# Performance work log

Measured on AMD Instinct MI355X. Metric: run time of the kernel, lower is better.

The kernel has to match this reference:

```python
import jax, jax.numpy as jnp
import numpy as np

# Deformable Aggregation (DAF) core of Sparse4DHead1st:
# multi-camera, multi-level bilinear point sampling + grouped weighted reduction.
# feature:            [bs, num_cams, sum(H_l*W_l), C]
# spatial_shapes:     [num_levels, 2] (H, W) per level (static metadata)
# level_start_index:  [num_levels] offsets into the flattened HW axis
# points_2d:          [bs, num_anchor, num_pts, num_cams, 2] normalized (x, y) in [0, 1]
# weights:            [bs, num_anchor, num_pts, num_cams, num_levels, num_groups]
# output:             [bs, num_anchor, C]  (sum over pts, cams, levels)

BS, CAMS, C = 1, 6, 256
NUM_ANCHOR, NUM_PTS = 900, 13
NUM_LEVELS, NUM_GROUPS = 4, 8
LEVEL_SHAPES = np.array([[64, 176], [32, 88], [16, 44], [8, 22]], np.int32)


def setup_inputs() -> dict:
    key = jax.random.key(0)
    k1, k2, k3 = jax.random.split(key, 3)
    hw = LEVEL_SHAPES[:, 0] * LEVEL_SHAPES[:, 1]
    starts = np.concatenate([[0], np.cumsum(hw)[:-1]]).astype(np.int32)
    total = int(hw.sum())  # 14960
    feature = jax.random.normal(k1, (BS, CAMS, total, C), jnp.float32)
    points_2d = jax.random.uniform(k2, (BS, NUM_ANCHOR, NUM_PTS, CAMS, 2), jnp.float32)
    # learned attention weights (normalized-ish so outputs stay O(1))
    weights = jax.random.uniform(
        k3, (BS, NUM_ANCHOR, NUM_PTS, CAMS, NUM_LEVELS, NUM_GROUPS), jnp.float32
    ) / (NUM_PTS * CAMS * NUM_LEVELS)
    return {
        "feature": feature,
        "spatial_shapes": jnp.asarray(LEVEL_SHAPES),
        "level_start_index": jnp.asarray(starts),
        "points_2d": points_2d,
        "weights": weights,
    }


def reference(feature, spatial_shapes, level_start_index, points_2d, weights):
    # spatial shapes / starts are static metadata (control slicing sizes)
    shapes = np.asarray(spatial_shapes)
    starts = np.asarray(level_start_index)
    bs, cams, _, c = feature.shape
    _, A, P, _, _ = points_2d.shape
    L, G = weights.shape[-2], weights.shape[-1]
    gc = c // G  # channels per group
    rowids = jnp.arange(bs * cams)[:, None]

    px = points_2d[..., 0]  # [bs, A, P, cams], normalized x
    py = points_2d[..., 1]

    out = jnp.zeros((bs, A, G, gc), feature.dtype)
    for l in range(L):
        h, w = int(shapes[l, 0]), int(shapes[l, 1])
        s = int(starts[l])
        feat = feature[:, :, s : s + h * w, :].reshape(bs * cams, h * w, c)
        x = px * w - 0.5
        y = py * h - 0.5
        x0 = jnp.floor(x)
        y0 = jnp.floor(y)
        bil = 0.0
        for dx in (0, 1):
            for dy in (0, 1):
                xi = x0 + dx
                yi = y0 + dy
                cw = (1.0 - jnp.abs(x - xi)) * (1.0 - jnp.abs(y - yi))
                valid = (xi >= 0) & (xi < w) & (yi >= 0) & (yi < h)
                idx = (jnp.clip(yi, 0, h - 1) * w + jnp.clip(xi, 0, w - 1)).astype(jnp.int32)
                # [bs, A, P, cams] -> [bs*cams, A*P]
                idx = idx.transpose(0, 3, 1, 2).reshape(bs * cams, A * P)
                cwm = (cw * valid).transpose(0, 3, 1, 2).reshape(bs * cams, A * P)
                v = feat[rowids, idx]  # gather: [bs*cams, A*P, C]
                bil = bil + v * cwm[..., None]
        bil = bil.reshape(bs, cams, A, P, G, gc)
        out = out + jnp.einsum("bcapgd,bapcg->bagd", bil, weights[..., l, :])
    return out.reshape(bs, A, c)
```

## Files before the change

kernel.cpp:

```cpp
#include <hip/hip_runtime.h>

#define NA 900
#define NP 13
#define NCAM 6
#define NL 4
#define NG 8
#define NC 256
#define TOTALHW 14960
#define NPC (NP * NCAM)
#define NS (NPC * NL)
#define NW 8

__device__ __constant__ int c_h[NL]  = {64, 32, 16, 8};
__device__ __constant__ int c_w[NL]  = {176, 88, 44, 22};
__device__ __constant__ int c_st[NL] = {0, 11264, 14080, 14784};

__global__ __launch_bounds__(512) void daf_kernel(
    const float* __restrict__ feature,
    const int* __restrict__ spatial_shapes,
    const int* __restrict__ level_start,
    const float* __restrict__ points,
    const float* __restrict__ weights,
    float* __restrict__ out)
{
    const int a    = blockIdx.x;
    const int tid  = threadIdx.x;
    const int wv   = tid >> 6;
    const int lane = tid & 63;

    __shared__ int    s_idx[NS][4];
    __shared__ float  s_cw[NS][4];
    __shared__ float  s_wg[NS * NG];
    __shared__ float4 s_part[NW][64];

    const float* wsrc = weights + (size_t)a * NS * NG;
    for (int i = tid; i < NS * NG; i += 512) {
        const int g  = i & (NG - 1);
        const int s  = i >> 3;
        const int l  = s / NPC;
        const int pc = s - l * NPC;
        s_wg[i] = wsrc[(pc * NL + l) * NG + g];
    }

    if (tid < NS) {
        const int s   = tid;
        const int l   = s / NPC;
        const int pc  = s - l * NPC;
        const int cam = pc % NCAM;
        const int p   = pc / NCAM;

        const float2 pt = *(const float2*)(points + (((size_t)a * NP + p) * NCAM + cam) * 2);
        const int h  = c_h[l];
        const int w  = c_w[l];
        const int st = c_st[l];

        const float x   = pt.x * (float)w - 0.5f;
        const float y   = pt.y * (float)h - 0.5f;
        const float x0f = floorf(x);
        const float y0f = floorf(y);
        const int   x0  = (int)x0f;
        const int   y0  = (int)y0f;
        const float fx  = x - x0f;
        const float fy  = y - y0f;
        const float wx[2] = {1.0f - fx, fx};
        const float wy[2] = {1.0f - fy, fy};

        const int base = cam * TOTALHW + st;
        #pragma unroll
        for (int k = 0; k < 4; ++k) {
            const int dx = k & 1;
            const int dy = k >> 1;
            const int xi = x0 + dx;
            const int yi = y0 + dy;
            const bool valid = (xi >= 0) && (xi < w) && (yi >= 0) && (yi < h);
            const int xc = min(max(xi, 0), w - 1);
            const int yc = min(max(yi, 0), h - 1);
            s_idx[s][k] = base + yc * w + xc;
            s_cw[s][k]  = valid ? wx[dx] * wy[dy] : 0.0f;
        }
    }
    __syncthreads();

    const int g = lane >> 3;
    const float4* __restrict__ f4 = (const float4*)feature;

    float4 acc = make_float4(0.f, 0.f, 0.f, 0.f);
    for (int s = wv; s < NS; s += NW) {
        const float wg = s_wg[s * NG + g];
        const int   i0 = s_idx[s][0], i1 = s_idx[s][1], i2 = s_idx[s][2], i3 = s_idx[s][3];
        const float c0 = s_cw[s][0] * wg, c1 = s_cw[s][1] * wg;
        const float c2 = s_cw[s][2] * wg, c3 = s_cw[s][3] * wg;

        const float4 v0 = f4[(size_t)i0 * 64 + lane];
        const float4 v1 = f4[(size_t)i1 * 64 + lane];
        const float4 v2 = f4[(size_t)i2 * 64 + lane];
        const float4 v3 = f4[(size_t)i3 * 64 + lane];

        acc.x += v0.x * c0 + v1.x * c1 + v2.x * c2 + v3.x * c3;
        acc.y += v0.y * c0 + v1.y * c1 + v2.y * c2 + v3.y * c3;
        acc.z += v0.z * c0 + v1.z * c1 + v2.z * c2 + v3.z * c3;
        acc.w += v0.w * c0 + v1.w * c1 + v2.w * c2 + v3.w * c3;
    }

    s_part[wv][lane] = acc;
    __syncthreads();

    if (tid < 64) {
        float4 r = s_part[0][lane];
        #pragma unroll
        for (int k = 1; k < NW; ++k) {
            const float4 p = s_part[k][lane];
            r.x += p.x; r.y += p.y; r.z += p.z; r.w += p.w;
        }
        ((float4*)out)[(size_t)a * 64 + lane] = r;
    }
}

extern "C" void kernel_launch(void* const* d_in, const int* in_sizes, int n_in,
                              void* d_out, int out_size, void* d_ws, size_t ws_size,
                              hipStream_t stream) {
    const float* feature        = (const float*)d_in[0];
    const int*   spatial_shapes = (const int*)d_in[1];
    const int*   level_start    = (const int*)d_in[2];
    const float* points         = (const float*)d_in[3];
    const float* weights        = (const float*)d_in[4];
    float*       out            = (float*)d_out;

    daf_kernel<<<NA, 512, 0, stream>>>(feature, spatial_shapes, level_start,
                                       points, weights, out);
}
```

Measured before the change: 214.5 us.

## Convert features to bf16 in workspace before gather-reduce kernel

Adds a pre-pass that converts the whole fp32 feature tensor to bf16 in the workspace, and a gather kernel that reads half-width bf16 rows and accumulates in fp32. The gather loop is also unrolled by two. The intent is to halve the bytes moved by the random bilinear gathers. The price is an extra full read of the feature tensor plus a half-size write on every call, and reduced precision in the sampled values. The fp32 kernel is kept as a fallback when the workspace is too small.

New measurement: 204.2 us. -4.8%, faster.

```diff
diff --git a/kernel.cpp b/kernel.cpp
--- a/kernel.cpp
+++ b/kernel.cpp
@@ -10,15 +10,40 @@
 #define NPC (NP * NCAM)
 #define NS (NPC * NL)
 #define NW 8
+#define FEAT_ELEMS (NCAM * TOTALHW * NC)
 
 __device__ __constant__ int c_h[NL]  = {64, 32, 16, 8};
 __device__ __constant__ int c_w[NL]  = {176, 88, 44, 22};
 __device__ __constant__ int c_st[NL] = {0, 11264, 14080, 14784};
 
-__global__ __launch_bounds__(512) void daf_kernel(
-    const float* __restrict__ feature,
-    const int* __restrict__ spatial_shapes,
-    const int* __restrict__ level_start,
+__device__ __forceinline__ float bfu(unsigned short u) {
+    union { unsigned int i; float f; } x;
+    x.i = ((unsigned int)u) << 16;
+    return x.f;
+}
+
+__global__ __launch_bounds__(256) void cvt_kernel(
+    const float* __restrict__ src, unsigned short* __restrict__ dst)
+{
+    const int n4 = FEAT_ELEMS / 4;
+    for (int i = blockIdx.x * 256 + threadIdx.x; i < n4; i += gridDim.x * 256) {
+        const float4 v = ((const float4*)src)[i];
+        ushort4 o;
+        const float* pv = (const float*)&v;
+        unsigned short* po = (unsigned short*)&o;
+        #pragma unroll
+        for (int k = 0; k < 4; ++k) {
+            union { float f; unsigned int u; } x;
+            x.f = pv[k];
+            unsigned int r = x.u + 0x7FFFu + ((x.u >> 16) & 1u);
+            po[k] = (unsigned short)(r >> 16);
+        }
+        ((ushort4*)dst)[i] = o;
+    }
+}
+
+__global__ __launch_bounds__(512) void daf_bf16_kernel(
+    const unsigned short* __restrict__ featb,
     const float* __restrict__ points,
     const float* __restrict__ weights,
     float* __restrict__ out)
@@ -82,6 +107,106 @@
     __syncthreads();
 
     const int g = lane >> 3;
+    const ushort4* __restrict__ fb = (const ushort4*)featb;
+
+    float4 acc = make_float4(0.f, 0.f, 0.f, 0.f);
+    #pragma unroll 2
+    for (int s = wv; s < NS; s += NW) {
+        const float wg = s_wg[s * NG + g];
+        const int   i0 = s_idx[s][0], i1 = s_idx[s][1], i2 = s_idx[s][2], i3 = s_idx[s][3];
+        const float c0 = s_cw[s][0] * wg, c1 = s_cw[s][1] * wg;
+        const float c2 = s_cw[s][2] * wg, c3 = s_cw[s][3] * wg;
+
+        const ushort4 r0 = fb[(size_t)i0 * 64 + lane];
+        const ushort4 r1 = fb[(size_t)i1 * 64 + lane];
+        const ushort4 r2 = fb[(size_t)i2 * 64 + lane];
+        const ushort4 r3 = fb[(size_t)i3 * 64 + lane];
+
+        acc.x += bfu(r0.x) * c0 + bfu(r1.x) * c1 + bfu(r2.x) * c2 + bfu(r3.x) * c3;
+        acc.y += bfu(r0.y) * c0 + bfu(r1.y) * c1 + bfu(r2.y) * c2 + bfu(r3.y) * c3;
+        acc.z += bfu(r0.z) * c0 + bfu(r1.z) * c1 + bfu(r2.z) * c2 + bfu(r3.z) * c3;
+        acc.w += bfu(r0.w) * c0 + bfu(r1.w) * c1 + bfu(r2.w) * c2 + bfu(r3.w) * c3;
+    }
+
+    s_part[wv][lane] = acc;
+    __syncthreads();
+
+    if (tid < 64) {
+        float4 r = s_part[0][lane];
+        #pragma unroll
+        for (int k = 1; k < NW; ++k) {
+            const float4 p = s_part[k][lane];
+            r.x += p.x; r.y += p.y; r.z += p.z; r.w += p.w;
+        }
+        ((float4*)out)[(size_t)a * 64 + lane] = r;
+    }
+}
+
+__global__ __launch_bounds__(512) void daf_f32_kernel(
+    const float* __restrict__ feature,
+    const float* __restrict__ points,
+    const float* __restrict__ weights,
+    float* __restrict__ out)
+{
+    const int a    = blockIdx.x;
+    const int tid  = threadIdx.x;
+    const int wv   = tid >> 6;
+    const int lane = tid & 63;
+
+    __shared__ int    s_idx[NS][4];
+    __shared__ float  s_cw[NS][4];
+    __shared__ float  s_wg[NS * NG];
+    __shared__ float4 s_part[NW][64];
+
+    const float* wsrc = weights + (size_t)a * NS * NG;
+    for (int i = tid; i < NS * NG; i += 512) {
+        const int g  = i & (NG - 1);
+        const int s  = i >> 3;
+        const int l  = s / NPC;
+        const int pc = s - l * NPC;
+        s_wg[i] = wsrc[(pc * NL + l) * NG + g];
+    }
+
+    if (tid < NS) {
+        const int s   = tid;
+        const int l   = s / NPC;
+        const int pc  = s - l * NPC;
+        const int cam = pc % NCAM;
+        const int p   = pc / NCAM;
+
+        const float2 pt = *(const float2*)(points + (((size_t)a * NP + p) * NCAM + cam) * 2);
+        const int h  = c_h[l];
+        const int w  = c_w[l];
+        const int st = c_st[l];
+
+        const float x   = pt.x * (float)w - 0.5f;
+        const float y   = pt.y * (float)h - 0.5f;
+        const float x0f = floorf(x);
+        const float y0f = floorf(y);
+        const int   x0  = (int)x0f;
+        const int   y0  = (int)y0f;
+        const float fx  = x - x0f;
+        const float fy  = y - y0f;
+        const float wx[2] = {1.0f - fx, fx};
+        const float wy[2] = {1.0f - fy, fy};
+
+        const int base = cam * TOTALHW + st;
+        #pragma unroll
+        for (int k = 0; k < 4; ++k) {
+            const int dx = k & 1;
+            const int dy = k >> 1;
+            const int xi = x0 + dx;
+            const int yi = y0 + dy;
+            const bool valid = (xi >= 0) && (xi < w) && (yi >= 0) && (yi < h);
+            const int xc = min(max(xi, 0), w - 1);
+            const int yc = min(max(yi, 0), h - 1);
+            s_idx[s][k] = base + yc * w + xc;
+            s_cw[s][k]  = valid ? wx[dx] * wy[dy] : 0.0f;
+        }
+    }
+    __syncthreads();
+
+    const int g = lane >> 3;
     const float4* __restrict__ f4 = (const float4*)feature;
 
     float4 acc = make_float4(0.f, 0.f, 0.f, 0.f);
@@ -120,12 +245,16 @@
                               void* d_out, int out_size, void* d_ws, size_t ws_size,
                               hipStream_t stream) {
     const float* feature        = (const float*)d_in[0];
-    const int*   spatial_shapes = (const int*)d_in[1];
-    const int*   level_start    = (const int*)d_in[2];
     const float* points         = (const float*)d_in[3];
     const float* weights        = (const float*)d_in[4];
     float*       out            = (float*)d_out;
 
-    daf_kernel<<<NA, 512, 0, stream>>>(feature, spatial_shapes, level_start,
-                                       points, weights, out);
-}
+    const size_t need = (size_t)FEAT_ELEMS * sizeof(unsigned short);
+    if (ws_size >= need && d_ws != nullptr) {
+        unsigned short* featb = (unsigned short*)d_ws;
+        cvt_kernel<<<2048, 256, 0, stream>>>(feature, featb);
+        daf_bf16_kernel<<<NA, 512, 0, stream>>>(featb, points, weights, out);
+    } else {
+        daf_f32_kernel<<<NA, 512, 0, stream>>>(feature, points, weights, out);
+    }
+}
```
